# Optimization experiments

Measured on AMD Instinct MI355X. Metric: run time of the kernel, lower is better.

Reference implementation:

```python
import jax, jax.numpy as jnp
import numpy as np

D_MODEL = 2048
N_HEADS = 16
D_K = D_MODEL // N_HEADS
D_FF = ((int(D_MODEL * 8 / 3) + 63) // 64) * 64  # 5504
B, S = 2, 2048
EPS = 1e-6


def setup_inputs() -> dict:
    key = jax.random.key(0)
    ks = jax.random.split(key, 16)
    sc = 0.02
    x = jax.random.normal(ks[0], (B, S, D_MODEL), dtype=jnp.float32)
    mask = jnp.tril(jnp.ones((S, S), dtype=jnp.int32))[None]  # [1,S,S] causal
    inp = {
        'x': x,
        'mask': mask,
        'wq': jax.random.normal(ks[1], (D_MODEL, D_MODEL), jnp.float32) * sc,
        'bq': jnp.zeros((D_MODEL,), jnp.float32),
        'wk': jax.random.normal(ks[2], (D_MODEL, D_MODEL), jnp.float32) * sc,
        'bk': jnp.zeros((D_MODEL,), jnp.float32),
        'wv': jax.random.normal(ks[3], (D_MODEL, D_MODEL), jnp.float32) * sc,
        'bv': jnp.zeros((D_MODEL,), jnp.float32),
        'wo': jax.random.normal(ks[4], (D_MODEL, D_MODEL), jnp.float32) * sc,
        'bo': jnp.zeros((D_MODEL,), jnp.float32),
        'g1': jnp.ones((D_MODEL,), jnp.float32),  # RMSNorm weights
        'g2': jnp.ones((D_MODEL,), jnp.float32),
        'w1': jax.random.normal(ks[5], (D_MODEL, D_FF), jnp.float32) * sc,
        'w3': jax.random.normal(ks[6], (D_MODEL, D_FF), jnp.float32) * sc,
        'w2': jax.random.normal(ks[7], (D_FF, D_MODEL), jnp.float32) * sc,
    }
    return inp


def _rmsnorm(x, w):
    rms = jnp.sqrt(jnp.mean(x * x, axis=-1, keepdims=True) + EPS)
    return x / rms * w


def _block(x, mask, wq, bq, wk, bk, wv, bv, wo, bo, g1, g2, w1, w2, w3):
    b, s, _ = x.shape
    # --- attention sublayer (pre-LN) ---
    n = _rmsnorm(x, g1)
    q = (n @ wq + bq).reshape(b, s, N_HEADS, D_K).transpose(0, 2, 1, 3)
    k = (n @ wk + bk).reshape(b, s, N_HEADS, D_K).transpose(0, 2, 1, 3)
    v = (n @ wv + bv).reshape(b, s, N_HEADS, D_K).transpose(0, 2, 1, 3)
    scores = jnp.einsum('bhqd,bhkd->bhqk', q, k) / jnp.sqrt(jnp.float32(D_K))
    m = mask[:, None, :, :]  # [1,1,S,S]
    scores = jnp.where(m == 0, jnp.float32(-jnp.inf), scores)
    attn = jax.nn.softmax(scores, axis=-1)
    ao = jnp.einsum('bhqk,bhkd->bhqd', attn, v)
    ao = ao.transpose(0, 2, 1, 3).reshape(b, s, D_MODEL)
    x = x + (ao @ wo + bo)
    # --- SwiGLU FFN sublayer (pre-LN) ---
    n = _rmsnorm(x, g2)
    ffn = (jax.nn.silu(n @ w1) * (n @ w3)) @ w2
    return x + ffn


def reference(x, mask, wq, bq, wk, bk, wv, bv, wo, bo, g1, g2, w1, w2, w3):
    return _block(x, mask, wq, bq, wk, bk, wv, bv, wo, bo, g1, g2, w1, w2, w3)
```

## Files before the change

kernel.cpp:

```cpp
#include <hip/hip_runtime.h>
#include <stdint.h>

typedef unsigned short u16;
typedef __bf16 bf16x8 __attribute__((ext_vector_type(8)));
typedef float f32x4 __attribute__((ext_vector_type(4)));

#define D_MODEL 2048
#define NHEADS 16
#define DK 128
#define DFF 5504
#define DFFP 5632
#define BB 2
#define SS 2048
#define MTOK 4096
#define DQKV 6144

#define AS1 __attribute__((address_space(1)))
#define AS3 __attribute__((address_space(3)))

__device__ __forceinline__ u16 f2bf(float f){
  union { float f; uint32_t u; } v; v.f = f;
  uint32_t r = v.u + 0x7fffu + ((v.u >> 16) & 1u);
  return (u16)(r >> 16);
}
__device__ __forceinline__ float bf2f(u16 u){
  union { uint32_t u; float f; } v; v.u = ((uint32_t)u) << 16;
  return v.f;
}
__device__ __forceinline__ u16 cvt_bf16(float f){
  union { __bf16 h; u16 u; } v; v.h = (__bf16)f; return v.u;
}
__device__ __forceinline__ float fexp2(float x){
#if __has_builtin(__builtin_amdgcn_exp2f)
  return __builtin_amdgcn_exp2f(x);
#else
  return exp2f(x);
#endif
}

__global__ __launch_bounds__(256) void k_transpose_w(const float* __restrict__ W,
                                                     u16* __restrict__ Wt, int K, int Nsrc){
  __shared__ float tile[32][33];
  int n0 = blockIdx.x * 32, k0 = blockIdx.y * 32;
  int tx = threadIdx.x, ty = threadIdx.y;
  #pragma unroll
  for (int r = 0; r < 4; ++r){
    int n = n0 + tx;
    tile[ty + r*8][tx] = (n < Nsrc) ? W[(size_t)(k0 + ty + r*8) * Nsrc + n] : 0.0f;
  }
  __syncthreads();
  #pragma unroll
  for (int r = 0; r < 4; ++r)
    Wt[(size_t)(n0 + ty + r*8) * K + k0 + tx] = f2bf(tile[tx][ty + r*8]);
}

__global__ __launch_bounds__(256) void k_transpose_w4(
    const float* __restrict__ w0s, const float* __restrict__ w1s,
    const float* __restrict__ w2s, const float* __restrict__ w3s,
    u16* __restrict__ d0, u16* __restrict__ d1,
    u16* __restrict__ d2, u16* __restrict__ d3){
  __shared__ float tile[32][33];
  const float* W = blockIdx.z == 0 ? w0s : blockIdx.z == 1 ? w1s : blockIdx.z == 2 ? w2s : w3s;
  u16* Wt = blockIdx.z == 0 ? d0 : blockIdx.z == 1 ? d1 : blockIdx.z == 2 ? d2 : d3;
  int n0 = blockIdx.x * 32, k0 = blockIdx.y * 32;
  int tx = threadIdx.x, ty = threadIdx.y;
  #pragma unroll
  for (int r = 0; r < 4; ++r)
    tile[ty + r*8][tx] = W[(size_t)(k0 + ty + r*8) * D_MODEL + n0 + tx];
  __syncthreads();
  #pragma unroll
  for (int r = 0; r < 4; ++r)
    Wt[(size_t)(n0 + ty + r*8) * D_MODEL + k0 + tx] = f2bf(tile[tx][ty + r*8]);
}

__global__ __launch_bounds__(256) void k_transpose_w13(
    const float* __restrict__ w1s, const float* __restrict__ w3s,
    u16* __restrict__ dst){
  __shared__ float tile[32][33];
  const float* W = blockIdx.z == 0 ? w1s : w3s;
  u16* Wt = dst + (size_t)blockIdx.z * DFFP * D_MODEL;
  int n0 = blockIdx.x * 32, k0 = blockIdx.y * 32;
  int tx = threadIdx.x, ty = threadIdx.y;
  #pragma unroll
  for (int r = 0; r < 4; ++r){
    int n = n0 + tx;
    tile[ty + r*8][tx] = (n < DFF) ? W[(size_t)(k0 + ty + r*8) * DFF + n] : 0.0f;
  }
  __syncthreads();
  #pragma unroll
  for (int r = 0; r < 4; ++r)
    Wt[(size_t)(n0 + ty + r*8) * D_MODEL + k0 + tx] = f2bf(tile[tx][ty + r*8]);
}

__global__ __launch_bounds__(256) void k_transpose_v(const u16* __restrict__ V,
                                                     u16* __restrict__ Vt, int ld){
  __shared__ u16 tile[32][33];
  int s0 = blockIdx.x * 32;
  int bh = blockIdx.y >> 2, dt = blockIdx.y & 3;
  int b = bh >> 4, h = bh & 15;
  int tx = threadIdx.x, ty = threadIdx.y;
  #pragma unroll
  for (int r = 0; r < 4; ++r)
    tile[ty + r*8][tx] = V[(size_t)(b*SS + s0 + ty + r*8) * ld + h*DK + dt*32 + tx];
  __syncthreads();
  #pragma unroll
  for (int r = 0; r < 4; ++r)
    Vt[(size_t)(bh*DK + dt*32 + ty + r*8) * SS + s0 + tx] = tile[tx][ty + r*8];
}

__global__ __launch_bounds__(256) void k_concat3(const float* __restrict__ a,
                                                 const float* __restrict__ b,
                                                 const float* __restrict__ c,
                                                 float* __restrict__ o){
  int i = blockIdx.x*256 + threadIdx.x;
  if (i >= DQKV) return;
  o[i] = (i < 2048) ? a[i] : (i < 4096 ? b[i-2048] : c[i-4096]);
}

__global__ __launch_bounds__(256) void k_rmsnorm(const float* __restrict__ X,
                                                 const float* __restrict__ g,
                                                 u16* __restrict__ out){
  int row = blockIdx.x, tid = threadIdx.x;
  const float* x = X + (size_t)row * D_MODEL;
  float4 a = ((const float4*)x)[tid*2];
  float4 b = ((const float4*)x)[tid*2+1];
  float ss = a.x*a.x + a.y*a.y + a.z*a.z + a.w*a.w
           + b.x*b.x + b.y*b.y + b.z*b.z + b.w*b.w;
  #pragma unroll
  for (int m = 1; m < 64; m <<= 1) ss += __shfl_xor(ss, m, 64);
  __shared__ float red[4];
  if ((tid & 63) == 0) red[tid >> 6] = ss;
  __syncthreads();
  float tot = red[0] + red[1] + red[2] + red[3];
  float sc = rsqrtf(tot * (1.0f / D_MODEL) + 1e-6f);
  float4 ga = ((const float4*)g)[tid*2];
  float4 gb = ((const float4*)g)[tid*2+1];
  uint32_t w0 = f2bf(a.x*sc*ga.x) | ((uint32_t)f2bf(a.y*sc*ga.y) << 16);
  uint32_t w1 = f2bf(a.z*sc*ga.z) | ((uint32_t)f2bf(a.w*sc*ga.w) << 16);
  uint32_t w2 = f2bf(b.x*sc*gb.x) | ((uint32_t)f2bf(b.y*sc*gb.y) << 16);
  uint32_t w3 = f2bf(b.z*sc*gb.z) | ((uint32_t)f2bf(b.w*sc*gb.w) << 16);
  ((uint4*)(out + (size_t)row * D_MODEL))[tid] = make_uint4(w0, w1, w2, w3);
}

__global__ __launch_bounds__(256) void k_addres_rms(
    const float* __restrict__ X, const float* __restrict__ bias,
    const float* __restrict__ p0, const float* __restrict__ p1,
    const float* __restrict__ g, float* __restrict__ out,
    u16* __restrict__ nrm){
  int row = blockIdx.x, tid = threadIdx.x;
  size_t base = (size_t)row * D_MODEL;
  float4 a  = ((const float4*)(X  + base))[tid*2];
  float4 b  = ((const float4*)(X  + base))[tid*2+1];
  float4 ba = ((const float4*)bias)[tid*2];
  float4 bb = ((const float4*)bias)[tid*2+1];
  float4 pa = ((const float4*)(p0 + base))[tid*2];
  float4 pb = ((const float4*)(p0 + base))[tid*2+1];
  float4 qa = ((const float4*)(p1 + base))[tid*2];
  float4 qb = ((const float4*)(p1 + base))[tid*2+1];
  a.x += ba.x + pa.x + qa.x; a.y += ba.y + pa.y + qa.y;
  a.z += ba.z + pa.z + qa.z; a.w += ba.w + pa.w + qa.w;
  b.x += bb.x + pb.x + qb.x; b.y += bb.y + pb.y + qb.y;
  b.z += bb.z + pb.z + qb.z; b.w += bb.w + pb.w + qb.w;
  ((float4*)(out + base))[tid*2]   = a;
  ((float4*)(out + base))[tid*2+1] = b;
  float ss = a.x*a.x + a.y*a.y + a.z*a.z + a.w*a.w
           + b.x*b.x + b.y*b.y + b.z*b.z + b.w*b.w;
  #pragma unroll
  for (int m = 1; m < 64; m <<= 1) ss += __shfl_xor(ss, m, 64);
  __shared__ float red[4];
  if ((tid & 63) == 0) red[tid >> 6] = ss;
  __syncthreads();
  float tot = red[0] + red[1] + red[2] + red[3];
  float sc = rsqrtf(tot * (1.0f / D_MODEL) + 1e-6f);
  float4 ga = ((const float4*)g)[tid*2];
  float4 gb = ((const float4*)g)[tid*2+1];
  uint32_t w0 = f2bf(a.x*sc*ga.x) | ((uint32_t)f2bf(a.y*sc*ga.y) << 16);
  uint32_t w1 = f2bf(a.z*sc*ga.z) | ((uint32_t)f2bf(a.w*sc*ga.w) << 16);
  uint32_t w2 = f2bf(b.x*sc*gb.x) | ((uint32_t)f2bf(b.y*sc*gb.y) << 16);
  uint32_t w3 = f2bf(b.z*sc*gb.z) | ((uint32_t)f2bf(b.w*sc*gb.w) << 16);
  ((uint4*)(nrm + base))[tid] = make_uint4(w0, w1, w2, w3);
}

__global__ __launch_bounds__(256) void k_silu_mul(const u16* __restrict__ a,
                                                  const u16* __restrict__ b,
                                                  u16* __restrict__ o, int n8){
  int i = blockIdx.x * 256 + threadIdx.x;
  if (i >= n8) return;
  uint4 av = ((const uint4*)a)[i];
  uint4 bv = ((const uint4*)b)[i];
  uint32_t aa[4] = {av.x, av.y, av.z, av.w};
  uint32_t bb[4] = {bv.x, bv.y, bv.z, bv.w};
  uint32_t rr[4];
  #pragma unroll
  for (int j = 0; j < 4; ++j){
    float x0 = bf2f((u16)(aa[j] & 0xffff)), x1 = bf2f((u16)(aa[j] >> 16));
    float y0 = bf2f((u16)(bb[j] & 0xffff)), y1 = bf2f((u16)(bb[j] >> 16));
    float r0 = x0 / (1.f + __expf(-x0)) * y0;
    float r1 = x1 / (1.f + __expf(-x1)) * y1;
    rr[j] = f2bf(r0) | ((uint32_t)f2bf(r1) << 16);
  }
  ((uint4*)o)[i] = make_uint4(rr[0], rr[1], rr[2], rr[3]);
}

template<int EPI>
__global__ __launch_bounds__(512, 2) void k_gemm8p(
    const u16* __restrict__ A, const u16* __restrict__ Bt,
    const float* __restrict__ bias, const u16* __restrict__ aux,
    void* __restrict__ Cout, int M, int N, int K,
    int lda, int ldb, int ldc)
{
  extern __shared__ __align__(16) char smem[];
  const int tid = threadIdx.x;
  const int lane = tid & 63, wid = tid >> 6;
  const int wr = wid >> 2, wc = wid & 3;
  const int lrow = lane & 15, lhi = lane >> 4;

  int nwg = gridDim.x, wg = blockIdx.x;
  int ksl = 0;
  if constexpr (EPI == 6 || EPI == 7){
    int hn = nwg >> 1;
    if (wg >= hn){ ksl = 1; wg -= hn; }
    nwg = hn;
    A  += (size_t)ksl * K;
    Bt += (size_t)ksl * K;
  }

  int nbx = N >> 8, nbm = M >> 8;
  int xcd = wg & 7, sub = wg >> 3;
  int m0, n0;
  if ((nwg & 7) == 0 && (nbm & 1) == 0 && (nbx & 3) == 0){
    int mh = nbm >> 1;
    int mr = sub % mh, nc = sub / mh;
    m0 = (((xcd & 1) * mh) + mr) << 8;
    n0 = (((xcd >> 1) * (nbx >> 2)) + nc) << 8;
  } else {
    int qq = nwg >> 3, rr2 = nwg & 7;
    int swz = (xcd < rr2 ? xcd*(qq+1) : rr2*(qq+1) + (xcd-rr2)*qq) + sub;
    m0 = (swz / nbx) << 8; n0 = (swz % nbx) << 8;
  }

  const int nk = K >> 6;
  const int hA = wr, hB = wc >> 1;
  const int gA = wc;
  const int gB = (wr << 1) | (wc & 1);

  const u16* aSrc[2][2]; int aDst[2][2];
  const u16* bSrc[2][2]; int bDst[2][2];
  #pragma unroll
  for (int q = 0; q < 2; ++q)
    #pragma unroll
    for (int L = 0; L < 2; ++L){
      int p = q*8192 + gA*2048 + L*1024 + lane*16;
      int row = p >> 7;
      int o = (p & 127) ^ ((row & 7) << 4);
      aSrc[q][L] = A + (size_t)(m0 + hA*128 + row)*lda + (o >> 1);
      aDst[q][L] = hA*16384 + p;
      int pb = q*4096 + (gB >> 1)*8192 + (gB & 1)*2048 + L*1024 + lane*16;
      int rowb = pb >> 7;
      int ob = (pb & 127) ^ ((rowb & 7) << 4);
      bSrc[q][L] = Bt + (size_t)(n0 + hB*128 + rowb)*ldb + (ob >> 1);
      bDst[q][L] = 32768 + hB*16384 + pb;
    }
  const int xo0 = (lhi*16) ^ ((lrow & 7) << 4);
  const int xo1 = (64 + lhi*16) ^ ((lrow & 7) << 4);

  auto stA = [&](int d, int kk, int q){
    #pragma unroll
    for (int L = 0; L < 2; ++L)
      __builtin_amdgcn_global_load_lds(
        (const AS1 void*)(aSrc[q][L] + kk),
        (AS3 void*)(smem + d*65536 + aDst[q][L]), 16, 0, 0);
  };
  auto stB = [&](int d, int kk, int s){
    #pragma unroll
    for (int L = 0; L < 2; ++L)
      __builtin_amdgcn_global_load_lds(
        (const AS1 void*)(bSrc[s][L] + kk),
        (AS3 void*)(smem + d*65536 + bDst[s][L]), 16, 0, 0);
  };
  auto rdA = [&](int d, int rloc, int ks)->bf16x8{
    return *(const bf16x8*)(smem + d*65536 + hA*16384 + rloc*128 + (ks ? xo1 : xo0));
  };
  auto rdB = [&](int d, int rloc, int ks)->bf16x8{
    return *(const bf16x8*)(smem + d*65536 + 32768 + hB*16384 + rloc*128 + (ks ? xo1 : xo0));
  };

  f32x4 acc[8][4] = {};

  stA(0, 0, 0); stB(0, 0, 0); stB(0, 0, 1); stA(0, 0, 1);
  asm volatile("s_waitcnt vmcnt(0)" ::: "memory");
  __builtin_amdgcn_s_barrier();

  for (int t = 0; t < nk; ++t){
    int d = t & 1, dn = d ^ 1, kkn = (t + 1) << 6;
    bool pf = (t + 1 < nk);
    bf16x8 aR[8], bQ0[4], bQ1[4];

    #pragma unroll
    for (int ii = 0; ii < 4; ++ii){
      aR[ii*2]   = rdA(d, ii*16 + lrow, 0);
      aR[ii*2+1] = rdA(d, ii*16 + lrow, 1);
    }
    #pragma unroll
    for (int j = 0; j < 2; ++j){
      bQ0[j*2]   = rdB(d, (wc&1)*64 + j*16 + lrow, 0);
      bQ0[j*2+1] = rdB(d, (wc&1)*64 + j*16 + lrow, 1);
    }
    if (pf) stA(dn, kkn, 0);
    __builtin_amdgcn_s_barrier();
    asm volatile("s_waitcnt lgkmcnt(0)" ::: "memory");
    __builtin_amdgcn_sched_barrier(0);
    __builtin_amdgcn_s_setprio(1);
    #pragma unroll
    for (int ii = 0; ii < 4; ++ii)
      #pragma unroll
      for (int j = 0; j < 2; ++j){
        acc[ii][j] = __builtin_amdgcn_mfma_f32_16x16x32_bf16(aR[ii*2],   bQ0[j*2],   acc[ii][j], 0, 0, 0);
        acc[ii][j] = __builtin_amdgcn_mfma_f32_16x16x32_bf16(aR[ii*2+1], bQ0[j*2+1], acc[ii][j], 0, 0, 0);
      }
    __builtin_amdgcn_s_setprio(0);
    if (pf) asm volatile("s_waitcnt vmcnt(4)" ::: "memory");
    else    asm volatile("s_waitcnt vmcnt(2)" ::: "memory");
    __builtin_amdgcn_sched_barrier(0);
    __builtin_amdgcn_s_barrier();

    #pragma unroll
    for (int j = 0; j < 2; ++j){
      bQ1[j*2]   = rdB(d, (wc&1)*64 + 32 + j*16 + lrow, 0);
      bQ1[j*2+1] = rdB(d, (wc&1)*64 + 32 + j*16 + lrow, 1);
    }
    if (pf) stB(dn, kkn, 0);
    __builtin_amdgcn_s_barrier();
    asm volatile("s_waitcnt lgkmcnt(0)" ::: "memory");
    __builtin_amdgcn_sched_barrier(0);
    __builtin_amdgcn_s_setprio(1);
    #pragma unroll
    for (int ii = 0; ii < 4; ++ii)
      #pragma unroll
      for (int j = 0; j < 2; ++j){
        acc[ii][2+j] = __builtin_amdgcn_mfma_f32_16x16x32_bf16(aR[ii*2],   bQ1[j*2],   acc[ii][2+j], 0, 0, 0);
        acc[ii][2+j] = __builtin_amdgcn_mfma_f32_16x16x32_bf16(aR[ii*2+1], bQ1[j*2+1], acc[ii][2+j], 0, 0, 0);
      }
    __builtin_amdgcn_s_setprio(0);
    if (pf) asm volatile("s_waitcnt vmcnt(4)" ::: "memory");
    else    asm volatile("s_waitcnt vmcnt(0)" ::: "memory");
    __builtin_amdgcn_sched_barrier(0);
    __builtin_amdgcn_s_barrier();

    #pragma unroll
    for (int ii = 0; ii < 4; ++ii){
      aR[ii*2]   = rdA(d, 64 + ii*16 + lrow, 0);
      aR[ii*2+1] = rdA(d, 64 + ii*16 + lrow, 1);
    }
    if (pf) stB(dn, kkn, 1);
    __builtin_amdgcn_s_barrier();
    asm volatile("s_waitcnt lgkmcnt(0)" ::: "memory");
    __builtin_amdgcn_sched_barrier(0);
    __builtin_amdgcn_s_setprio(1);
    #pragma unroll
    for (int ii = 0; ii < 4; ++ii)
      #pragma unroll
      for (int j = 0; j < 2; ++j){
        acc[4+ii][2+j] = __builtin_amdgcn_mfma_f32_16x16x32_bf16(aR[ii*2],   bQ1[j*2],   acc[4+ii][2+j], 0, 0, 0);
        acc[4+ii][2+j] = __builtin_amdgcn_mfma_f32_16x16x32_bf16(aR[ii*2+1], bQ1[j*2+1], acc[4+ii][2+j], 0, 0, 0);
      }
    __builtin_amdgcn_s_setprio(0);
    __builtin_amdgcn_s_barrier();

    if (pf) stA(dn, kkn, 1);
    __builtin_amdgcn_s_setprio(1);
    #pragma unroll
    for (int ii = 0; ii < 4; ++ii)
      #pragma unroll
      for (int j = 0; j < 2; ++j){
        acc[4+ii][j] = __builtin_amdgcn_mfma_f32_16x16x32_bf16(aR[ii*2],   bQ0[j*2],   acc[4+ii][j], 0, 0, 0);
        acc[4+ii][j] = __builtin_amdgcn_mfma_f32_16x16x32_bf16(aR[ii*2+1], bQ0[j*2+1], acc[4+ii][j], 0, 0, 0);
      }
    __builtin_amdgcn_s_setprio(0);
    if (pf) asm volatile("s_waitcnt vmcnt(4)" ::: "memory");
    __builtin_amdgcn_sched_barrier(0);
    __builtin_amdgcn_s_barrier();
  }

  if constexpr (EPI == 6){
    float* P = ksl ? (float*)aux : (float*)Cout;
    #pragma unroll
    for (int i = 0; i < 8; ++i)
      #pragma unroll
      for (int j = 0; j < 4; ++j){
        int col = n0 + wc*64 + j*16 + lrow;
        #pragma unroll
        for (int q = 0; q < 4; ++q){
          int row = m0 + wr*128 + i*16 + lhi*4 + q;
          P[(size_t)row*ldc + col] = acc[i][j][q];
        }
      }
    return;
  }
  if constexpr (EPI == 7){
    float* P = (float*)Cout;
    #pragma unroll
    for (int i = 0; i < 8; ++i)
      #pragma unroll
      for (int j = 0; j < 4; ++j){
        int col = n0 + wc*64 + j*16 + lrow;
        #pragma unroll
        for (int q = 0; q < 4; ++q){
          int row = m0 + wr*128 + i*16 + lhi*4 + q;
          atomicAdd(P + (size_t)row*ldc + col, acc[i][j][q]);
        }
      }
    return;
  }
  u16* Cw = (u16*)Cout;
  int cofs = 0;
  if constexpr (EPI == 5){
    if (n0 >= 5632){ Cw = (u16*)aux; cofs = 5632; }
  }
  #pragma unroll
  for (int i = 0; i < 8; ++i){
    #pragma unroll
    for (int j = 0; j < 4; ++j){
      int col = n0 + wc*64 + j*16 + lrow;
      float bv = 0.f;
      if constexpr (EPI == 0) bv = bias[col];
      #pragma unroll
      for (int q = 0; q < 4; ++q){
        int row = m0 + wr*128 + i*16 + lhi*4 + q;
        float v = acc[i][j][q] + bv;
        Cw[(size_t)row*ldc + (col - cofs)] = f2bf(v);
      }
    }
  }
}

template<int EPI>
__global__ __launch_bounds__(256) void k_gemm_bt(
    const u16* __restrict__ A, const u16* __restrict__ Bt,
    const float* __restrict__ bias, const float* __restrict__ res,
    const u16* __restrict__ aux,
    void* __restrict__ Cout, int M, int N, int K,
    int lda, int ldb, int ldc)
{
  __shared__ __align__(16) u16 As[3][128*32];
  __shared__ __align__(16) u16 Bs[3][128*32];
  int tid = threadIdx.x;

  int nwg = gridDim.x, wg = blockIdx.x;
  int qq = nwg >> 3, rr = nwg & 7;
  int xcd = wg & 7, sub = wg >> 3;
  int swz = (xcd < rr ? xcd*(qq+1) : rr*(qq+1) + (xcd-rr)*qq) + sub;
  int nbx = N >> 7;
  int m0 = (swz / nbx) << 7, n0 = (swz % nbx) << 7;

  int lane = tid & 63, wave = tid >> 6;
  int wr = wave >> 1, wc = wave & 1;
  int lrow = lane & 15, lhi = lane >> 4;
  f32x4 acc[4][4] = {};
  int srow = tid >> 2;
  int schk = tid & 3;
  const int nk = K >> 5;

  auto stage = [&](int slot, int kt){
    int k0 = kt << 5;
    int c = schk ^ (srow & 3);
    #pragma unroll
    for (int cc = 0; cc < 2; ++cc){
      int r = cc*64 + srow;
      __builtin_amdgcn_global_load_lds(
        (const AS1 void*)(A + (size_t)(m0 + r)*lda + k0 + c*8),
        (AS3 void*)(&As[slot][r*32 + schk*8]), 16, 0, 0);
      __builtin_amdgcn_global_load_lds(
        (const AS1 void*)(Bt + (size_t)(n0 + r)*ldb + k0 + c*8),
        (AS3 void*)(&Bs[slot][r*32 + schk*8]), 16, 0, 0);
    }
  };

  stage(0, 0);
  if (nk > 1) stage(1, 1);
  if (nk > 1) asm volatile("s_waitcnt vmcnt(4)" ::: "memory");
  else        asm volatile("s_waitcnt vmcnt(0)" ::: "memory");
  __builtin_amdgcn_s_barrier();

  for (int kt = 0; kt < nk; ++kt){
    int cur = kt % 3;
    if (kt + 2 < nk) stage((kt + 2) % 3, kt + 2);
    int rchk = lhi ^ (lrow & 3);
    bf16x8 af[4], bfv[4];
    #pragma unroll
    for (int i = 0; i < 4; ++i){
      af[i]  = *(const bf16x8*)(&As[cur][(wr*64 + i*16 + lrow)*32 + rchk*8]);
      bfv[i] = *(const bf16x8*)(&Bs[cur][(wc*64 + i*16 + lrow)*32 + rchk*8]);
    }
    #pragma unroll
    for (int i = 0; i < 4; ++i)
      #pragma unroll
      for (int j = 0; j < 4; ++j)
        acc[i][j] = __builtin_amdgcn_mfma_f32_16x16x32_bf16(af[i], bfv[j], acc[i][j], 0, 0, 0);
    if (kt + 2 < nk) asm volatile("s_waitcnt vmcnt(4)" ::: "memory");
    else             asm volatile("s_waitcnt vmcnt(0)" ::: "memory");
    __builtin_amdgcn_s_barrier();
  }

  #pragma unroll
  for (int i = 0; i < 4; ++i){
    #pragma unroll
    for (int j = 0; j < 4; ++j){
      int col = n0 + wc*64 + j*16 + lrow;
      float bv = 0.f;
      if constexpr (EPI == 0 || EPI == 1) bv = bias[col];
      #pragma unroll
      for (int q = 0; q < 4; ++q){
        int row = m0 + wr*64 + i*16 + lhi*4 + q;
        size_t idx = (size_t)row*ldc + col;
        float v = acc[i][j][q] + bv;
        if constexpr (EPI == 1 || EPI == 3) v += res[idx];
        if constexpr (EPI == 4){
          float a0 = bf2f(aux[idx]);
          v = a0 / (1.f + __expf(-a0)) * v;
        }
        if constexpr (EPI == 0 || EPI == 2 || EPI == 4) ((u16*)Cout)[idx] = f2bf(v);
        else ((float*)Cout)[idx] = v;
      }
    }
  }
}

__global__ __launch_bounds__(512) void k_attn(
    const u16* __restrict__ Q, const u16* __restrict__ Kb,
    const u16* __restrict__ Vt, u16* __restrict__ O, int ldq)
{
  int tid = threadIdx.x, lane = tid & 63, wave = tid >> 6;
  int lrow = lane & 15, lhi = lane >> 4;
  int bidx = blockIdx.x;
  int bh = bidx >> 3, j = bidx & 7;
  int b = bh >> 4, h = bh & 15;

  __shared__ __align__(16) u16 Kbuf[2][64*128];
  __shared__ __align__(16) u16 Vbuf[2][128*64];
  __shared__ __align__(16) u16 P_lds[8][16*64];
  char* pw = (char*)&P_lds[wave][0];
  const float sc2 = 0.08838834764831845f * 1.44269504088896340736f;

  auto stage = [&](int bufi, int kt){
    int kv0 = kt << 6;
    char* kd = (char*)&Kbuf[bufi][0];
    char* vd = (char*)&Vbuf[bufi][0];
    #pragma unroll
    for (int L = 0; L < 2; ++L){
      int cid = wave*128 + L*64 + lane;
      int r = cid >> 4, c = cid & 15;
      int cg = c ^ (r & 7);
      __builtin_amdgcn_global_load_lds(
        (const AS1 void*)(Kb + (size_t)(b*SS + kv0 + r)*ldq + h*DK + cg*8),
        (AS3 void*)(kd + wave*2048 + L*1024 + lane*16), 16, 0, 0);
      int dd = cid >> 3, c8 = cid & 7;
      int cv = c8 ^ (dd & 7);
      __builtin_amdgcn_global_load_lds(
        (const AS1 void*)(Vt + (size_t)bh*DK*SS + (size_t)dd*SS + kv0 + cv*8),
        (AS3 void*)(vd + wave*2048 + L*1024 + lane*16), 16, 0, 0);
    }
  };

  #pragma unroll 1
  for (int item = 0; item < 2; ++item){
    int qi = item == 0 ? 15 - j : j;
    int qs = qi * 128;
    int nt = 2*qi + 2;
    int qrow = qs + wave * 16;

    bf16x8 qf[4];
    const u16* qbase = Q + (size_t)(b*SS + qrow + lrow)*ldq + h*DK + lhi*8;
    #pragma unroll
    for (int dc = 0; dc < 4; ++dc) qf[dc] = *(const bf16x8*)(qbase + dc*32);

    f32x4 accO[8] = {};
    float mr[4] = {-1e30f,-1e30f,-1e30f,-1e30f};
    float lr[4] = {0.f,0.f,0.f,0.f};

    stage(0, 0);
    __syncthreads();

    for (int kt = 0; kt < nt; ++kt){
      int cur = kt & 1;
      if (kt + 1 < nt) stage(cur ^ 1, kt + 1);
      int kv0 = kt << 6;
      if (kv0 <= qrow + 15){
        const char* kl = (const char*)&Kbuf[cur][0];
        const char* vl = (const char*)&Vbuf[cur][0];
        bool domask = (kv0 + 63 > qrow);

        f32x4 sf[4];
        #pragma unroll
        for (int hf = 0; hf < 4; ++hf){
          int rl = hf*16 + lrow;
          int sw = rl & 7;
          f32x4 a = {};
          #pragma unroll
          for (int dc = 0; dc < 4; ++dc){
            bf16x8 kf = *(const bf16x8*)(kl + rl*256 + (((lhi + dc*4) ^ sw) << 4));
            a = __builtin_amdgcn_mfma_f32_16x16x32_bf16(qf[dc], kf, a, 0, 0, 0);
          }
          sf[hf] = a;
        }

        float p[4][4], mx[4];
        #pragma unroll
        for (int q = 0; q < 4; ++q){
          float s0 = sf[0][q]*sc2, s1 = sf[1][q]*sc2, s2 = sf[2][q]*sc2, s3 = sf[3][q]*sc2;
          if (domask){
            int qg = qrow + lhi*4 + q;
            if (kv0      + lrow > qg) s0 = -1e30f;
            if (kv0 + 16 + lrow > qg) s1 = -1e30f;
            if (kv0 + 32 + lrow > qg) s2 = -1e30f;
            if (kv0 + 48 + lrow > qg) s3 = -1e30f;
          }
          p[q][0]=s0; p[q][1]=s1; p[q][2]=s2; p[q][3]=s3;
          float m = fmaxf(fmaxf(s0,s1), fmaxf(s2,s3));
          m = fmaxf(m, __shfl_xor(m, 1, 64));
          m = fmaxf(m, __shfl_xor(m, 2, 64));
          m = fmaxf(m, __shfl_xor(m, 4, 64));
          m = fmaxf(m, __shfl_xor(m, 8, 64));
          mx[q] = m;
        }
        float dmax = fmaxf(fmaxf(mx[0]-mr[0], mx[1]-mr[1]), fmaxf(mx[2]-mr[2], mx[3]-mr[3]));
        bool rescale = !__all(dmax <= 8.0f);
        float al[4];
        #pragma unroll
        for (int q = 0; q < 4; ++q){
          if (rescale){
            float mn = fmaxf(mr[q], mx[q]);
            al[q] = fexp2(mr[q] - mn);
            mr[q] = mn;
          } else al[q] = 1.0f;
          p[q][0] = fexp2(p[q][0] - mr[q]);
          p[q][1] = fexp2(p[q][1] - mr[q]);
          p[q][2] = fexp2(p[q][2] - mr[q]);
          p[q][3] = fexp2(p[q][3] - mr[q]);
          float sm = (p[q][0] + p[q][1]) + (p[q][2] + p[q][3]);
          sm += __shfl_xor(sm, 1, 64);
          sm += __shfl_xor(sm, 2, 64);
          sm += __shfl_xor(sm, 4, 64);
          sm += __shfl_xor(sm, 8, 64);
          lr[q] = lr[q]*al[q] + sm;
        }
        if (rescale){
          #pragma unroll
          for (int f = 0; f < 8; ++f)
            #pragma unroll
            for (int q = 0; q < 4; ++q) accO[f][q] *= al[q];
        }

        #pragma unroll
        for (int q = 0; q < 4; ++q){
          int row = lhi*4 + q;
          int rb = row*128, sw = (row & 7) << 4;
          #pragma unroll
          for (int hf = 0; hf < 4; ++hf)
            *(u16*)(pw + rb + ((hf*32 + lrow*2) ^ sw)) = cvt_bf16(p[q][hf]);
        }
        __builtin_amdgcn_sched_barrier(0);
        int rsw = (lrow & 7) << 4;
        bf16x8 pa0 = *(const bf16x8*)(pw + lrow*128 + ((     lhi*16) ^ rsw));
        bf16x8 pa1 = *(const bf16x8*)(pw + lrow*128 + ((64 + lhi*16) ^ rsw));

        #pragma unroll
        for (int f = 0; f < 8; ++f){
          int d = f*16 + lrow;
          int swv = d & 7;
          bf16x8 v0 = *(const bf16x8*)(vl + d*128 + (((lhi    ) ^ swv) << 4));
          bf16x8 v1 = *(const bf16x8*)(vl + d*128 + (((lhi + 4) ^ swv) << 4));
          accO[f] = __builtin_amdgcn_mfma_f32_16x16x32_bf16(pa0, v0, accO[f], 0, 0, 0);
          accO[f] = __builtin_amdgcn_mfma_f32_16x16x32_bf16(pa1, v1, accO[f], 0, 0, 0);
        }
      }
      __syncthreads();
    }

    #pragma unroll
    for (int q = 0; q < 4; ++q){
      float inv = 1.0f / lr[q];
      #pragma unroll
      for (int f = 0; f < 8; ++f){
        int row = b*SS + qrow + lhi*4 + q;
        int col = h*DK + f*16 + lrow;
        O[(size_t)row*D_MODEL + col] = cvt_bf16(accO[f][q] * inv);
      }
    }
    __syncthreads();
  }
}

extern "C" void kernel_launch(void* const* d_in, const int* in_sizes, int n_in,
                              void* d_out, int out_size, void* d_ws, size_t ws_size,
                              hipStream_t stream)
{
  (void)in_sizes; (void)n_in; (void)out_size;
  const float* x  = (const float*)d_in[0];
  const float* wq = (const float*)d_in[2];
  const float* bq = (const float*)d_in[3];
  const float* wk = (const float*)d_in[4];
  const float* bk = (const float*)d_in[5];
  const float* wv = (const float*)d_in[6];
  const float* bv = (const float*)d_in[7];
  const float* wo = (const float*)d_in[8];
  const float* bo = (const float*)d_in[9];
  const float* g1 = (const float*)d_in[10];
  const float* g2 = (const float*)d_in[11];
  const float* w1 = (const float*)d_in[12];
  const float* w3 = (const float*)d_in[13];
  const float* w2 = (const float*)d_in[14];
  float* out = (float*)d_out;

  const size_t MB = 1u << 20;
  const size_t W2T_B = (size_t)D_MODEL * DFF * sizeof(u16);
  const size_t NEED = 152*MB + W2T_B + 32768;
  if (ws_size < NEED) return;
  char* ws = (char*)d_ws;
  u16* bufA  = (u16*)(ws + 0);
  u16* qkv   = (u16*)(ws + 16*MB);
  u16* h1    = qkv;
  u16* wqkvt = (u16*)(ws + 64*MB);
  u16* w1w3t = (u16*)(ws + 64*MB);
  u16* wot   = (u16*)(ws + 88*MB);
  u16* vtb   = (u16*)(ws + 96*MB);
  u16* h3    = (u16*)(ws + 108*MB);
  float* p0o = (float*)(ws + 16*MB);
  float* p1o = (float*)(ws + 108*MB);
  u16* w2t   = (u16*)(ws + 152*MB);
  float* bqkv = (float*)(ws + 152*MB + W2T_B);

  bool big = true;
  big &= hipFuncSetAttribute((const void*)k_gemm8p<0>, hipFuncAttributeMaxDynamicSharedMemorySize, 131072) == hipSuccess;
  big &= hipFuncSetAttribute((const void*)k_gemm8p<5>, hipFuncAttributeMaxDynamicSharedMemorySize, 131072) == hipSuccess;
  big &= hipFuncSetAttribute((const void*)k_gemm8p<6>, hipFuncAttributeMaxDynamicSharedMemorySize, 131072) == hipSuccess;
  big &= hipFuncSetAttribute((const void*)k_gemm8p<7>, hipFuncAttributeMaxDynamicSharedMemorySize, 131072) == hipSuccess;

  dim3 tb(32, 8);
  k_transpose_w4<<<dim3(64,64,4), tb, 0, stream>>>(wq, wk, wv, wo,
      wqkvt, wqkvt + 2048*2048, wqkvt + 2*2048*2048, wot);
  k_transpose_w<<<dim3(64, DFF/32), tb, 0, stream>>>(w2, w2t, DFF, D_MODEL);
  k_concat3<<<24, 256, 0, stream>>>(bq, bk, bv, bqkv);

  k_rmsnorm<<<MTOK, 256, 0, stream>>>(x, g1, bufA);
  if (big){
    k_gemm8p<0><<<(MTOK/256)*(DQKV/256), 512, 131072, stream>>>(bufA, wqkvt, bqkv, nullptr, qkv, MTOK, DQKV, D_MODEL, D_MODEL, D_MODEL, DQKV);
    k_transpose_v<<<dim3(SS/32, 128), tb, 0, stream>>>(qkv + 4096, vtb, DQKV);
    k_attn<<<dim3(BB*NHEADS*8), 512, 0, stream>>>(qkv, qkv + 2048, vtb, bufA, DQKV);
    k_gemm8p<6><<<2*(MTOK/256)*(D_MODEL/256), 512, 131072, stream>>>(bufA, wot, nullptr, (const u16*)p1o, p0o, MTOK, D_MODEL, D_MODEL/2, D_MODEL, D_MODEL, D_MODEL);
    k_transpose_w13<<<dim3(DFFP/32, 64, 2), tb, 0, stream>>>(w1, w3, w1w3t);
    k_addres_rms<<<MTOK, 256, 0, stream>>>(x, bo, p0o, p1o, g2, out, bufA);
    k_gemm8p<5><<<(MTOK/256)*((2*DFFP)/256), 512, 131072, stream>>>(bufA, w1w3t, nullptr, h3, h1, MTOK, 2*DFFP, D_MODEL, D_MODEL, D_MODEL, DFFP);
    k_silu_mul<<<(MTOK*DFFP/8 + 255)/256, 256, 0, stream>>>(h1, h3, h1, MTOK*DFFP/8);
    k_gemm8p<7><<<2*(MTOK/256)*(D_MODEL/256), 512, 131072, stream>>>(h1, w2t, nullptr, nullptr, out, MTOK, D_MODEL, DFF/2, DFFP, DFF, D_MODEL);
  } else {
    k_gemm_bt<0><<<(DQKV/128)*(MTOK/128), 256, 0, stream>>>(bufA, wqkvt, bqkv, nullptr, nullptr, qkv, MTOK, DQKV, D_MODEL, D_MODEL, D_MODEL, DQKV);
    k_transpose_v<<<dim3(SS/32, 128), tb, 0, stream>>>(qkv + 4096, vtb, DQKV);
    k_transpose_w13<<<dim3(DFFP/32, 64, 2), tb, 0, stream>>>(w1, w3, w1w3t);
    k_attn<<<dim3(BB*NHEADS*8), 512, 0, stream>>>(qkv, qkv + 2048, vtb, bufA, DQKV);
    k_gemm_bt<1><<<16*32, 256, 0, stream>>>(bufA, wot, bo, x, nullptr, out, MTOK, D_MODEL, D_MODEL, D_MODEL, D_MODEL, D_MODEL);
    k_rmsnorm<<<MTOK, 256, 0, stream>>>(out, g2, bufA);
    k_gemm_bt<2><<<(DFFP/128)*32, 256, 0, stream>>>(bufA, w1w3t, nullptr, nullptr, nullptr, h1, MTOK, DFFP, D_MODEL, D_MODEL, D_MODEL, DFFP);
    k_gemm_bt<2><<<(DFFP/128)*32, 256, 0, stream>>>(bufA, w1w3t + (size_t)DFFP*2048, nullptr, nullptr, nullptr, h3, MTOK, DFFP, D_MODEL, D_MODEL, D_MODEL, DFFP);
    k_silu_mul<<<(MTOK*DFFP/8 + 255)/256, 256, 0, stream>>>(h1, h3, h1, MTOK*DFFP/8);
    k_gemm_bt<3><<<16*32, 256, 0, stream>>>(h1, w2t, nullptr, out, nullptr, out, MTOK, D_MODEL, DFF, DFFP, DFF, D_MODEL);
  }
}
```

Baseline: 686.8 us.

## Replace atomic split-K epilogue with partial buffers plus add kernel; reorder GEMM prefetch

The final FFN down-projection GEMM no longer uses atomicAdd to accumulate its two K-slices into the output. Each slice now writes plain fp32 partials to workspace, and a new elementwise kernel adds both partials into the residual output. The GEMM main loop is also restructured: the B-half-0 prefetch is issued together with A-half-0 and the MFMA/store phases are reordered, with the vmcnt waits raised to match. This trades atomic contention for an extra memory pass and kernel launch, and the reordering changes how much global-load latency is hidden.

Measured after the change: 666.0 us. 3.0% less time.

```diff
diff --git a/kernel.cpp b/kernel.cpp
--- a/kernel.cpp
+++ b/kernel.cpp
@@ -202,6 +202,19 @@
   ((uint4*)o)[i] = make_uint4(rr[0], rr[1], rr[2], rr[3]);
 }
 
+__global__ __launch_bounds__(256) void k_add2(float* __restrict__ out,
+                                              const float* __restrict__ p0,
+                                              const float* __restrict__ p1, int n4){
+  int stride = gridDim.x * 256;
+  for (int i = blockIdx.x * 256 + threadIdx.x; i < n4; i += stride){
+    float4 o = ((const float4*)out)[i];
+    float4 a = ((const float4*)p0)[i];
+    float4 b = ((const float4*)p1)[i];
+    o.x += a.x + b.x; o.y += a.y + b.y; o.z += a.z + b.z; o.w += a.w + b.w;
+    ((float4*)out)[i] = o;
+  }
+}
+
 template<int EPI>
 __global__ __launch_bounds__(512, 2) void k_gemm8p(
     const u16* __restrict__ A, const u16* __restrict__ Bt,
@@ -217,7 +230,7 @@
 
   int nwg = gridDim.x, wg = blockIdx.x;
   int ksl = 0;
-  if constexpr (EPI == 6 || EPI == 7){
+  if constexpr (EPI == 6){
     int hn = nwg >> 1;
     if (wg >= hn){ ksl = 1; wg -= hn; }
     nwg = hn;
@@ -306,7 +319,7 @@
       bQ0[j*2]   = rdB(d, (wc&1)*64 + j*16 + lrow, 0);
       bQ0[j*2+1] = rdB(d, (wc&1)*64 + j*16 + lrow, 1);
     }
-    if (pf) stA(dn, kkn, 0);
+    if (pf){ stA(dn, kkn, 0); stB(dn, kkn, 0); }
     __builtin_amdgcn_s_barrier();
     asm volatile("s_waitcnt lgkmcnt(0)" ::: "memory");
     __builtin_amdgcn_sched_barrier(0);
@@ -319,7 +332,7 @@
         acc[ii][j] = __builtin_amdgcn_mfma_f32_16x16x32_bf16(aR[ii*2+1], bQ0[j*2+1], acc[ii][j], 0, 0, 0);
       }
     __builtin_amdgcn_s_setprio(0);
-    if (pf) asm volatile("s_waitcnt vmcnt(4)" ::: "memory");
+    if (pf) asm volatile("s_waitcnt vmcnt(6)" ::: "memory");
     else    asm volatile("s_waitcnt vmcnt(2)" ::: "memory");
     __builtin_amdgcn_sched_barrier(0);
     __builtin_amdgcn_s_barrier();
@@ -328,29 +341,6 @@
     for (int j = 0; j < 2; ++j){
       bQ1[j*2]   = rdB(d, (wc&1)*64 + 32 + j*16 + lrow, 0);
       bQ1[j*2+1] = rdB(d, (wc&1)*64 + 32 + j*16 + lrow, 1);
-    }
-    if (pf) stB(dn, kkn, 0);
-    __builtin_amdgcn_s_barrier();
-    asm volatile("s_waitcnt lgkmcnt(0)" ::: "memory");
-    __builtin_amdgcn_sched_barrier(0);
-    __builtin_amdgcn_s_setprio(1);
-    #pragma unroll
-    for (int ii = 0; ii < 4; ++ii)
-      #pragma unroll
-      for (int j = 0; j < 2; ++j){
-        acc[ii][2+j] = __builtin_amdgcn_mfma_f32_16x16x32_bf16(aR[ii*2],   bQ1[j*2],   acc[ii][2+j], 0, 0, 0);
-        acc[ii][2+j] = __builtin_amdgcn_mfma_f32_16x16x32_bf16(aR[ii*2+1], bQ1[j*2+1], acc[ii][2+j], 0, 0, 0);
-      }
-    __builtin_amdgcn_s_setprio(0);
-    if (pf) asm volatile("s_waitcnt vmcnt(4)" ::: "memory");
-    else    asm volatile("s_waitcnt vmcnt(0)" ::: "memory");
-    __builtin_amdgcn_sched_barrier(0);
-    __builtin_amdgcn_s_barrier();
-
-    #pragma unroll
-    for (int ii = 0; ii < 4; ++ii){
-      aR[ii*2]   = rdA(d, 64 + ii*16 + lrow, 0);
-      aR[ii*2+1] = rdA(d, 64 + ii*16 + lrow, 1);
     }
     if (pf) stB(dn, kkn, 1);
     __builtin_amdgcn_s_barrier();
@@ -361,13 +351,35 @@
     for (int ii = 0; ii < 4; ++ii)
       #pragma unroll
       for (int j = 0; j < 2; ++j){
+        acc[ii][2+j] = __builtin_amdgcn_mfma_f32_16x16x32_bf16(aR[ii*2],   bQ1[j*2],   acc[ii][2+j], 0, 0, 0);
+        acc[ii][2+j] = __builtin_amdgcn_mfma_f32_16x16x32_bf16(aR[ii*2+1], bQ1[j*2+1], acc[ii][2+j], 0, 0, 0);
+      }
+    __builtin_amdgcn_s_setprio(0);
+    if (pf) asm volatile("s_waitcnt vmcnt(6)" ::: "memory");
+    else    asm volatile("s_waitcnt vmcnt(0)" ::: "memory");
+    __builtin_amdgcn_sched_barrier(0);
+    __builtin_amdgcn_s_barrier();
+
+    #pragma unroll
+    for (int ii = 0; ii < 4; ++ii){
+      aR[ii*2]   = rdA(d, 64 + ii*16 + lrow, 0);
+      aR[ii*2+1] = rdA(d, 64 + ii*16 + lrow, 1);
+    }
+    if (pf) stA(dn, kkn, 1);
+    __builtin_amdgcn_s_barrier();
+    asm volatile("s_waitcnt lgkmcnt(0)" ::: "memory");
+    __builtin_amdgcn_sched_barrier(0);
+    __builtin_amdgcn_s_setprio(1);
+    #pragma unroll
+    for (int ii = 0; ii < 4; ++ii)
+      #pragma unroll
+      for (int j = 0; j < 2; ++j){
         acc[4+ii][2+j] = __builtin_amdgcn_mfma_f32_16x16x32_bf16(aR[ii*2],   bQ1[j*2],   acc[4+ii][2+j], 0, 0, 0);
         acc[4+ii][2+j] = __builtin_amdgcn_mfma_f32_16x16x32_bf16(aR[ii*2+1], bQ1[j*2+1], acc[4+ii][2+j], 0, 0, 0);
       }
     __builtin_amdgcn_s_setprio(0);
     __builtin_amdgcn_s_barrier();
 
-    if (pf) stA(dn, kkn, 1);
     __builtin_amdgcn_s_setprio(1);
     #pragma unroll
     for (int ii = 0; ii < 4; ++ii)
@@ -393,21 +405,6 @@
         for (int q = 0; q < 4; ++q){
           int row = m0 + wr*128 + i*16 + lhi*4 + q;
           P[(size_t)row*ldc + col] = acc[i][j][q];
-        }
-      }
-    return;
-  }
-  if constexpr (EPI == 7){
-    float* P = (float*)Cout;
-    #pragma unroll
-    for (int i = 0; i < 8; ++i)
-      #pragma unroll
-      for (int j = 0; j < 4; ++j){
-        int col = n0 + wc*64 + j*16 + lrow;
-        #pragma unroll
-        for (int q = 0; q < 4; ++q){
-          int row = m0 + wr*128 + i*16 + lhi*4 + q;
-          atomicAdd(P + (size_t)row*ldc + col, acc[i][j][q]);
         }
       }
     return;
@@ -727,6 +724,8 @@
   u16* h3    = (u16*)(ws + 108*MB);
   float* p0o = (float*)(ws + 16*MB);
   float* p1o = (float*)(ws + 108*MB);
+  float* p0  = (float*)(ws + 64*MB);
+  float* p1  = (float*)(ws + 96*MB);
   u16* w2t   = (u16*)(ws + 152*MB);
   float* bqkv = (float*)(ws + 152*MB + W2T_B);
 
@@ -734,7 +733,6 @@
   big &= hipFuncSetAttribute((const void*)k_gemm8p<0>, hipFuncAttributeMaxDynamicSharedMemorySize, 131072) == hipSuccess;
   big &= hipFuncSetAttribute((const void*)k_gemm8p<5>, hipFuncAttributeMaxDynamicSharedMemorySize, 131072) == hipSuccess;
   big &= hipFuncSetAttribute((const void*)k_gemm8p<6>, hipFuncAttributeMaxDynamicSharedMemorySize, 131072) == hipSuccess;
-  big &= hipFuncSetAttribute((const void*)k_gemm8p<7>, hipFuncAttributeMaxDynamicSharedMemorySize, 131072) == hipSuccess;
 
   dim3 tb(32, 8);
   k_transpose_w4<<<dim3(64,64,4), tb, 0, stream>>>(wq, wk, wv, wo,
@@ -752,7 +750,8 @@
     k_addres_rms<<<MTOK, 256, 0, stream>>>(x, bo, p0o, p1o, g2, out, bufA);
     k_gemm8p<5><<<(MTOK/256)*((2*DFFP)/256), 512, 131072, stream>>>(bufA, w1w3t, nullptr, h3, h1, MTOK, 2*DFFP, D_MODEL, D_MODEL, D_MODEL, DFFP);
     k_silu_mul<<<(MTOK*DFFP/8 + 255)/256, 256, 0, stream>>>(h1, h3, h1, MTOK*DFFP/8);
-    k_gemm8p<7><<<2*(MTOK/256)*(D_MODEL/256), 512, 131072, stream>>>(h1, w2t, nullptr, nullptr, out, MTOK, D_MODEL, DFF/2, DFFP, DFF, D_MODEL);
+    k_gemm8p<6><<<2*(MTOK/256)*(D_MODEL/256), 512, 131072, stream>>>(h1, w2t, nullptr, (const u16*)p1, p0, MTOK, D_MODEL, DFF/2, DFFP, DFF, D_MODEL);
+    k_add2<<<2048, 256, 0, stream>>>(out, p0, p1, MTOK*D_MODEL/4);
   } else {
     k_gemm_bt<0><<<(DQKV/128)*(MTOK/128), 256, 0, stream>>>(bufA, wqkvt, bqkv, nullptr, nullptr, qkv, MTOK, DQKV, D_MODEL, D_MODEL, D_MODEL, DQKV);
     k_transpose_v<<<dim3(SS/32, 128), tb, 0, stream>>>(qkv + 4096, vtb, DQKV);
```

## Replace split-K output and FFN-down GEMMs with 256x128 tile kernel

Applied to the files above, without the earlier changes.

Drops the two-way split-K scheme (partial buffers and atomicAdd) for the attention output projection and the FFN down projection. Both now use a new GEMM kernel with 256x128 tiles, 96KB LDS and a direct fp32 store, with the residual add done in the epilogue. The main GEMM's prefetch order is also rearranged, with adjusted vmcnt waits. This removes atomics and the extra partial-sum traffic, at the cost of fewer blocks (256) on a 256-CU part and lower per-tile reuse, while the residual-RMS kernel skips the second partial read.

Result: faster. 655.8 us (-4.5%).

```diff
diff --git a/kernel.cpp b/kernel.cpp
--- a/kernel.cpp
+++ b/kernel.cpp
@@ -155,12 +155,16 @@
   float4 bb = ((const float4*)bias)[tid*2+1];
   float4 pa = ((const float4*)(p0 + base))[tid*2];
   float4 pb = ((const float4*)(p0 + base))[tid*2+1];
-  float4 qa = ((const float4*)(p1 + base))[tid*2];
-  float4 qb = ((const float4*)(p1 + base))[tid*2+1];
-  a.x += ba.x + pa.x + qa.x; a.y += ba.y + pa.y + qa.y;
-  a.z += ba.z + pa.z + qa.z; a.w += ba.w + pa.w + qa.w;
-  b.x += bb.x + pb.x + qb.x; b.y += bb.y + pb.y + qb.y;
-  b.z += bb.z + pb.z + qb.z; b.w += bb.w + pb.w + qb.w;
+  a.x += ba.x + pa.x; a.y += ba.y + pa.y;
+  a.z += ba.z + pa.z; a.w += ba.w + pa.w;
+  b.x += bb.x + pb.x; b.y += bb.y + pb.y;
+  b.z += bb.z + pb.z; b.w += bb.w + pb.w;
+  if (p1){
+    float4 qa = ((const float4*)(p1 + base))[tid*2];
+    float4 qb = ((const float4*)(p1 + base))[tid*2+1];
+    a.x += qa.x; a.y += qa.y; a.z += qa.z; a.w += qa.w;
+    b.x += qb.x; b.y += qb.y; b.z += qb.z; b.w += qb.w;
+  }
   ((float4*)(out + base))[tid*2]   = a;
   ((float4*)(out + base))[tid*2+1] = b;
   float ss = a.x*a.x + a.y*a.y + a.z*a.z + a.w*a.w
@@ -216,14 +220,6 @@
   const int lrow = lane & 15, lhi = lane >> 4;
 
   int nwg = gridDim.x, wg = blockIdx.x;
-  int ksl = 0;
-  if constexpr (EPI == 6 || EPI == 7){
-    int hn = nwg >> 1;
-    if (wg >= hn){ ksl = 1; wg -= hn; }
-    nwg = hn;
-    A  += (size_t)ksl * K;
-    Bt += (size_t)ksl * K;
-  }
 
   int nbx = N >> 8, nbm = M >> 8;
   int xcd = wg & 7, sub = wg >> 3;
@@ -306,7 +302,7 @@
       bQ0[j*2]   = rdB(d, (wc&1)*64 + j*16 + lrow, 0);
       bQ0[j*2+1] = rdB(d, (wc&1)*64 + j*16 + lrow, 1);
     }
-    if (pf) stA(dn, kkn, 0);
+    if (pf){ stA(dn, kkn, 0); stB(dn, kkn, 0); }
     __builtin_amdgcn_s_barrier();
     asm volatile("s_waitcnt lgkmcnt(0)" ::: "memory");
     __builtin_amdgcn_sched_barrier(0);
@@ -319,7 +315,7 @@
         acc[ii][j] = __builtin_amdgcn_mfma_f32_16x16x32_bf16(aR[ii*2+1], bQ0[j*2+1], acc[ii][j], 0, 0, 0);
       }
     __builtin_amdgcn_s_setprio(0);
-    if (pf) asm volatile("s_waitcnt vmcnt(4)" ::: "memory");
+    if (pf) asm volatile("s_waitcnt vmcnt(6)" ::: "memory");
     else    asm volatile("s_waitcnt vmcnt(2)" ::: "memory");
     __builtin_amdgcn_sched_barrier(0);
     __builtin_amdgcn_s_barrier();
@@ -329,7 +325,7 @@
       bQ1[j*2]   = rdB(d, (wc&1)*64 + 32 + j*16 + lrow, 0);
       bQ1[j*2+1] = rdB(d, (wc&1)*64 + 32 + j*16 + lrow, 1);
     }
-    if (pf) stB(dn, kkn, 0);
+    if (pf) stB(dn, kkn, 1);
     __builtin_amdgcn_s_barrier();
     asm volatile("s_waitcnt lgkmcnt(0)" ::: "memory");
     __builtin_amdgcn_sched_barrier(0);
@@ -342,7 +338,7 @@
         acc[ii][2+j] = __builtin_amdgcn_mfma_f32_16x16x32_bf16(aR[ii*2+1], bQ1[j*2+1], acc[ii][2+j], 0, 0, 0);
       }
     __builtin_amdgcn_s_setprio(0);
-    if (pf) asm volatile("s_waitcnt vmcnt(4)" ::: "memory");
+    if (pf) asm volatile("s_waitcnt vmcnt(6)" ::: "memory");
     else    asm volatile("s_waitcnt vmcnt(0)" ::: "memory");
     __builtin_amdgcn_sched_barrier(0);
     __builtin_amdgcn_s_barrier();
@@ -352,7 +348,7 @@
       aR[ii*2]   = rdA(d, 64 + ii*16 + lrow, 0);
       aR[ii*2+1] = rdA(d, 64 + ii*16 + lrow, 1);
     }
-    if (pf) stB(dn, kkn, 1);
+    if (pf) stA(dn, kkn, 1);
     __builtin_amdgcn_s_barrier();
     asm volatile("s_waitcnt lgkmcnt(0)" ::: "memory");
     __builtin_amdgcn_sched_barrier(0);
@@ -367,7 +363,6 @@
     __builtin_amdgcn_s_setprio(0);
     __builtin_amdgcn_s_barrier();
 
-    if (pf) stA(dn, kkn, 1);
     __builtin_amdgcn_s_setprio(1);
     #pragma unroll
     for (int ii = 0; ii < 4; ++ii)
@@ -382,36 +377,6 @@
     __builtin_amdgcn_s_barrier();
   }
 
-  if constexpr (EPI == 6){
-    float* P = ksl ? (float*)aux : (float*)Cout;
-    #pragma unroll
-    for (int i = 0; i < 8; ++i)
-      #pragma unroll
-      for (int j = 0; j < 4; ++j){
-        int col = n0 + wc*64 + j*16 + lrow;
-        #pragma unroll
-        for (int q = 0; q < 4; ++q){
-          int row = m0 + wr*128 + i*16 + lhi*4 + q;
-          P[(size_t)row*ldc + col] = acc[i][j][q];
-        }
-      }
-    return;
-  }
-  if constexpr (EPI == 7){
-    float* P = (float*)Cout;
-    #pragma unroll
-    for (int i = 0; i < 8; ++i)
-      #pragma unroll
-      for (int j = 0; j < 4; ++j){
-        int col = n0 + wc*64 + j*16 + lrow;
-        #pragma unroll
-        for (int q = 0; q < 4; ++q){
-          int row = m0 + wr*128 + i*16 + lhi*4 + q;
-          atomicAdd(P + (size_t)row*ldc + col, acc[i][j][q]);
-        }
-      }
-    return;
-  }
   u16* Cw = (u16*)Cout;
   int cofs = 0;
   if constexpr (EPI == 5){
@@ -429,6 +394,161 @@
         int row = m0 + wr*128 + i*16 + lhi*4 + q;
         float v = acc[i][j][q] + bv;
         Cw[(size_t)row*ldc + (col - cofs)] = f2bf(v);
+      }
+    }
+  }
+}
+
+template<int EPI>
+__global__ __launch_bounds__(512, 2) void k_gemm8pn(
+    const u16* __restrict__ A, const u16* __restrict__ Bt,
+    const float* __restrict__ res, float* __restrict__ Cout,
+    int M, int N, int K, int lda, int ldb, int ldc)
+{
+  extern __shared__ __align__(16) char smem[];
+  const int tid = threadIdx.x;
+  const int lane = tid & 63, wid = tid >> 6;
+  const int wr = wid >> 2, wc = wid & 3;
+  const int lrow = lane & 15, lhi = lane >> 4;
+
+  int nwg = gridDim.x, wg = blockIdx.x;
+  int nbx = N >> 7, nbm = M >> 8;
+  int xcd = wg & 7, sub = wg >> 3;
+  int m0, n0;
+  if ((nwg & 7) == 0 && (nbm & 1) == 0 && (nbx & 3) == 0){
+    int mh = nbm >> 1;
+    int mr = sub % mh, nc = sub / mh;
+    m0 = (((xcd & 1) * mh) + mr) << 8;
+    n0 = (((xcd >> 1) * (nbx >> 2)) + nc) << 7;
+  } else {
+    int qq = nwg >> 3, rr2 = nwg & 7;
+    int swz = (xcd < rr2 ? xcd*(qq+1) : rr2*(qq+1) + (xcd-rr2)*qq) + sub;
+    m0 = (swz / nbx) << 8; n0 = (swz % nbx) << 7;
+  }
+
+  const int nk = K >> 6;
+  const int hA = wr;
+  const int gA = wc;
+
+  const u16* aSrc[2][2]; int aDst[2][2];
+  #pragma unroll
+  for (int q = 0; q < 2; ++q)
+    #pragma unroll
+    for (int L = 0; L < 2; ++L){
+      int p = q*8192 + gA*2048 + L*1024 + lane*16;
+      int row = p >> 7;
+      int o = (p & 127) ^ ((row & 7) << 4);
+      aSrc[q][L] = A + (size_t)(m0 + hA*128 + row)*lda + (o >> 1);
+      aDst[q][L] = hA*16384 + p;
+    }
+  const u16* bSrc[2]; int bDst[2];
+  #pragma unroll
+  for (int s = 0; s < 2; ++s){
+    int p = s*8192 + wid*1024 + lane*16;
+    int row = p >> 7;
+    int o = (p & 127) ^ ((row & 7) << 4);
+    bSrc[s] = Bt + (size_t)(n0 + row)*ldb + (o >> 1);
+    bDst[s] = 32768 + p;
+  }
+  const int xo0 = (lhi*16) ^ ((lrow & 7) << 4);
+  const int xo1 = (64 + lhi*16) ^ ((lrow & 7) << 4);
+
+  auto stA = [&](int d, int kk, int q){
+    #pragma unroll
+    for (int L = 0; L < 2; ++L)
+      __builtin_amdgcn_global_load_lds(
+        (const AS1 void*)(aSrc[q][L] + kk),
+        (AS3 void*)(smem + d*49152 + aDst[q][L]), 16, 0, 0);
+  };
+  auto stB = [&](int d, int kk){
+    #pragma unroll
+    for (int s = 0; s < 2; ++s)
+      __builtin_amdgcn_global_load_lds(
+        (const AS1 void*)(bSrc[s] + kk),
+        (AS3 void*)(smem + d*49152 + bDst[s]), 16, 0, 0);
+  };
+  auto rdA = [&](int d, int rloc, int ks)->bf16x8{
+    return *(const bf16x8*)(smem + d*49152 + hA*16384 + rloc*128 + (ks ? xo1 : xo0));
+  };
+  auto rdB = [&](int d, int rloc, int ks)->bf16x8{
+    return *(const bf16x8*)(smem + d*49152 + 32768 + rloc*128 + (ks ? xo1 : xo0));
+  };
+
+  f32x4 acc[8][2] = {};
+
+  stA(0, 0, 0); stB(0, 0); stA(0, 0, 1);
+  asm volatile("s_waitcnt vmcnt(0)" ::: "memory");
+  __builtin_amdgcn_s_barrier();
+
+  for (int t = 0; t < nk; ++t){
+    int d = t & 1, dn = d ^ 1, kkn = (t + 1) << 6;
+    bool pf = (t + 1 < nk);
+    bf16x8 aR[8], bQ[4];
+
+    #pragma unroll
+    for (int ii = 0; ii < 4; ++ii){
+      aR[ii*2]   = rdA(d, ii*16 + lrow, 0);
+      aR[ii*2+1] = rdA(d, ii*16 + lrow, 1);
+    }
+    #pragma unroll
+    for (int j = 0; j < 2; ++j){
+      bQ[j*2]   = rdB(d, wc*32 + j*16 + lrow, 0);
+      bQ[j*2+1] = rdB(d, wc*32 + j*16 + lrow, 1);
+    }
+    if (pf){ stA(dn, kkn, 0); stB(dn, kkn); }
+    __builtin_amdgcn_s_barrier();
+    asm volatile("s_waitcnt lgkmcnt(0)" ::: "memory");
+    __builtin_amdgcn_sched_barrier(0);
+    __builtin_amdgcn_s_setprio(1);
+    #pragma unroll
+    for (int ii = 0; ii < 4; ++ii)
+      #pragma unroll
+      for (int j = 0; j < 2; ++j){
+        acc[ii][j] = __builtin_amdgcn_mfma_f32_16x16x32_bf16(aR[ii*2],   bQ[j*2],   acc[ii][j], 0, 0, 0);
+        acc[ii][j] = __builtin_amdgcn_mfma_f32_16x16x32_bf16(aR[ii*2+1], bQ[j*2+1], acc[ii][j], 0, 0, 0);
+      }
+    __builtin_amdgcn_s_setprio(0);
+    if (pf) asm volatile("s_waitcnt vmcnt(4)" ::: "memory");
+    else    asm volatile("s_waitcnt vmcnt(0)" ::: "memory");
+    __builtin_amdgcn_sched_barrier(0);
+    __builtin_amdgcn_s_barrier();
+
+    #pragma unroll
+    for (int ii = 0; ii < 4; ++ii){
+      aR[ii*2]   = rdA(d, 64 + ii*16 + lrow, 0);
+      aR[ii*2+1] = rdA(d, 64 + ii*16 + lrow, 1);
+    }
+    if (pf) stA(dn, kkn, 1);
+    __builtin_amdgcn_s_barrier();
+    asm volatile("s_waitcnt lgkmcnt(0)" ::: "memory");
+    __builtin_amdgcn_sched_barrier(0);
+    __builtin_amdgcn_s_setprio(1);
+    #pragma unroll
+    for (int ii = 0; ii < 4; ++ii)
+      #pragma unroll
+      for (int j = 0; j < 2; ++j){
+        acc[4+ii][j] = __builtin_amdgcn_mfma_f32_16x16x32_bf16(aR[ii*2],   bQ[j*2],   acc[4+ii][j], 0, 0, 0);
+        acc[4+ii][j] = __builtin_amdgcn_mfma_f32_16x16x32_bf16(aR[ii*2+1], bQ[j*2+1], acc[4+ii][j], 0, 0, 0);
+      }
+    __builtin_amdgcn_s_setprio(0);
+    if (pf) asm volatile("s_waitcnt vmcnt(2)" ::: "memory");
+    else    asm volatile("s_waitcnt vmcnt(0)" ::: "memory");
+    __builtin_amdgcn_sched_barrier(0);
+    __builtin_amdgcn_s_barrier();
+  }
+
+  #pragma unroll
+  for (int i = 0; i < 8; ++i){
+    #pragma unroll
+    for (int j = 0; j < 2; ++j){
+      int col = n0 + wc*32 + j*16 + lrow;
+      #pragma unroll
+      for (int q = 0; q < 4; ++q){
+        int row = m0 + wr*128 + i*16 + lhi*4 + q;
+        size_t idx = (size_t)row*ldc + col;
+        float v = acc[i][j][q];
+        if constexpr (EPI == 8) v += res[idx];
+        Cout[idx] = v;
       }
     }
   }
@@ -726,15 +846,14 @@
   u16* vtb   = (u16*)(ws + 96*MB);
   u16* h3    = (u16*)(ws + 108*MB);
   float* p0o = (float*)(ws + 16*MB);
-  float* p1o = (float*)(ws + 108*MB);
   u16* w2t   = (u16*)(ws + 152*MB);
   float* bqkv = (float*)(ws + 152*MB + W2T_B);
 
   bool big = true;
   big &= hipFuncSetAttribute((const void*)k_gemm8p<0>, hipFuncAttributeMaxDynamicSharedMemorySize, 131072) == hipSuccess;
   big &= hipFuncSetAttribute((const void*)k_gemm8p<5>, hipFuncAttributeMaxDynamicSharedMemorySize, 131072) == hipSuccess;
-  big &= hipFuncSetAttribute((const void*)k_gemm8p<6>, hipFuncAttributeMaxDynamicSharedMemorySize, 131072) == hipSuccess;
-  big &= hipFuncSetAttribute((const void*)k_gemm8p<7>, hipFuncAttributeMaxDynamicSharedMemorySize, 131072) == hipSuccess;
+  big &= hipFuncSetAttribute((const void*)k_gemm8pn<8>, hipFuncAttributeMaxDynamicSharedMemorySize, 98304) == hipSuccess;
+  big &= hipFuncSetAttribute((const void*)k_gemm8pn<9>, hipFuncAttributeMaxDynamicSharedMemorySize, 98304) == hipSuccess;
 
   dim3 tb(32, 8);
   k_transpose_w4<<<dim3(64,64,4), tb, 0, stream>>>(wq, wk, wv, wo,
@@ -747,12 +866,12 @@
     k_gemm8p<0><<<(MTOK/256)*(DQKV/256), 512, 131072, stream>>>(bufA, wqkvt, bqkv, nullptr, qkv, MTOK, DQKV, D_MODEL, D_MODEL, D_MODEL, DQKV);
     k_transpose_v<<<dim3(SS/32, 128), tb, 0, stream>>>(qkv + 4096, vtb, DQKV);
     k_attn<<<dim3(BB*NHEADS*8), 512, 0, stream>>>(qkv, qkv + 2048, vtb, bufA, DQKV);
-    k_gemm8p<6><<<2*(MTOK/256)*(D_MODEL/256), 512, 131072, stream>>>(bufA, wot, nullptr, (const u16*)p1o, p0o, MTOK, D_MODEL, D_MODEL/2, D_MODEL, D_MODEL, D_MODEL);
+    k_gemm8pn<9><<<(MTOK/256)*(D_MODEL/128), 512, 98304, stream>>>(bufA, wot, nullptr, p0o, MTOK, D_MODEL, D_MODEL, D_MODEL, D_MODEL, D_MODEL);
     k_transpose_w13<<<dim3(DFFP/32, 64, 2), tb, 0, stream>>>(w1, w3, w1w3t);
-    k_addres_rms<<<MTOK, 256, 0, stream>>>(x, bo, p0o, p1o, g2, out, bufA);
+    k_addres_rms<<<MTOK, 256, 0, stream>>>(x, bo, p0o, nullptr, g2, out, bufA);
     k_gemm8p<5><<<(MTOK/256)*((2*DFFP)/256), 512, 131072, stream>>>(bufA, w1w3t, nullptr, h3, h1, MTOK, 2*DFFP, D_MODEL, D_MODEL, D_MODEL, DFFP);
     k_silu_mul<<<(MTOK*DFFP/8 + 255)/256, 256, 0, stream>>>(h1, h3, h1, MTOK*DFFP/8);
-    k_gemm8p<7><<<2*(MTOK/256)*(D_MODEL/256), 512, 131072, stream>>>(h1, w2t, nullptr, nullptr, out, MTOK, D_MODEL, DFF/2, DFFP, DFF, D_MODEL);
+    k_gemm8pn<8><<<(MTOK/256)*(D_MODEL/128), 512, 98304, stream>>>(h1, w2t, out, out, MTOK, D_MODEL, DFF, DFFP, DFF, D_MODEL);
   } else {
     k_gemm_bt<0><<<(DQKV/128)*(MTOK/128), 256, 0, stream>>>(bufA, wqkvt, bqkv, nullptr, nullptr, qkv, MTOK, DQKV, D_MODEL, D_MODEL, D_MODEL, DQKV);
     k_transpose_v<<<dim3(SS/32, 128), tb, 0, stream>>>(qkv + 4096, vtb, DQKV);
```
